# Kernel optimization log

Measured on AMD Instinct MI355X. Metric: run time of the kernel, lower is better.

## Reference

```python
import jax, jax.numpy as jnp
import numpy as np

B, CLS, BBOX, H, W = 64, 80, 2, 56, 56
TOPK = 2048
L_COORD, L_OBJ, L_NOOBJ = 5.0, 1.0, 0.5


def setup_inputs() -> dict:
    key = jax.random.key(0)
    ks = jax.random.split(key, 5)
    pred_cls = jax.random.normal(ks[0], (B, CLS, H, W), jnp.float32)
    pred_response = jax.random.uniform(ks[1], (B, BBOX, H, W), jnp.float32)
    pred_bboxes = jax.random.uniform(ks[2], (B, BBOX * 4, H, W), jnp.float32)
    label_cls = jax.random.uniform(ks[3], (B, CLS, H, W), jnp.float32)
    label_bboxes = jax.random.uniform(ks[4], (B, BBOX * 4, H, W), jnp.float32)
    # exactly TOPK positive cells so the data-dependent k is static
    rng = np.random.default_rng(0)
    flat = rng.choice(B * H * W, size=TOPK, replace=False)
    lr = np.zeros((B, BBOX, H, W), np.float32)
    b = flat // (H * W); rem = flat % (H * W)
    lr[b, :, rem // W, rem % W] = 1.0
    return {
        'pred_cls': pred_cls, 'pred_response': pred_response, 'pred_bboxes': pred_bboxes,
        'label_cls': label_cls, 'label_response': jnp.asarray(lr), 'label_bboxes': label_bboxes,
        'topk': TOPK,
    }


def _offset2box(box):
    # box: [N,4] (cx, cy, w, h) -> (x1, y1, x2, y2)
    x1 = box[:, 0] - box[:, 2] / 2
    y1 = box[:, 1] - box[:, 3] / 2
    return jnp.stack([x1, y1, x1 + box[:, 2], y1 + box[:, 3]], axis=1)


def _paired_iou(box1, box2):
    # elementwise (paired) IoU: box1, box2 [N,4] in (x1,y1,x2,y2)
    lt = jnp.maximum(box1[:, :2], box2[:, :2])
    rb = jnp.minimum(box1[:, 2:], box2[:, 2:])
    wh = jnp.clip(rb - lt, 0.0)
    inter = wh[:, 0] * wh[:, 1]
    a1 = (box1[:, 2] - box1[:, 0]) * (box1[:, 3] - box1[:, 1])
    a2 = (box2[:, 2] - box2[:, 0]) * (box2[:, 3] - box2[:, 1])
    return inter / (a1 + a2 - inter + 1e-4)


def reference(pred_cls, pred_response, pred_bboxes, label_cls, label_response, label_bboxes, topk):
    b_size, _, h, w = pred_cls.shape
    bbox_num = pred_response.shape[1]

    # --- positive cell selection (no grad) ---
    tmp = label_response.sum(axis=1)            # [B,H,W]
    flat = jnp.where(tmp < 0.5, 0.0, tmp).reshape(-1)
    _, idx = jax.lax.top_k(flat, topk)          # static k
    hw = h * w
    b_list = idx // hw
    rem = idx % hw
    y_list = rem // w
    x_list = rem % w

    # --- gather positives: [K, C] each ---
    t_resp = label_response[b_list, :, y_list, x_list]
    p_resp = pred_response[b_list, :, y_list, x_list]
    t_boxes = label_bboxes[b_list, :, y_list, x_list]    # [K, bbox*4]
    p_boxes = pred_bboxes[b_list, :, y_list, x_list]
    t_cls = label_cls[b_list, :, y_list, x_list]
    p_cls = pred_cls[b_list, :, y_list, x_list]

    loss_pos_cls = jnp.sum((p_cls - t_cls) ** 2)

    # --- IoU between paired boxes (no grad in original) ---
    t_off = t_boxes.reshape(-1, 4)
    p_off = p_boxes.reshape(-1, 4)
    iou = _paired_iou(_offset2box(t_off), _offset2box(p_off)).reshape(-1, bbox_num)
    iou = jax.lax.stop_gradient(iou)

    best = jnp.argmax(iou, axis=1)[:, None]     # [K,1]
    p_best_resp = jnp.take_along_axis(p_resp, best, axis=1)
    iou_best = jnp.take_along_axis(iou, best, axis=1)
    loss_pos_response = jnp.sum((p_best_resp - iou_best) ** 2)

    p_b = p_boxes.reshape(-1, bbox_num, 4)
    t_b = t_boxes.reshape(-1, bbox_num, 4)
    off_idx = best[:, :, None]                  # [K,1,1]
    p_sel = jnp.take_along_axis(p_b, jnp.broadcast_to(off_idx, (p_b.shape[0], 1, 4)), axis=1)
    t_sel = jnp.take_along_axis(t_b, jnp.broadcast_to(off_idx, (t_b.shape[0], 1, 4)), axis=1)
    loss_pos_offset = jnp.sum((p_sel - t_sel) ** 2)

    # --- negatives over the full map ---
    neg_mask = label_response < 1.0
    loss_neg_response = jnp.sum(jnp.where(neg_mask, (pred_response - label_response) ** 2, 0.0))

    pObj = loss_pos_response / b_size * L_OBJ
    nObj = loss_neg_response / b_size * L_NOOBJ
    cls_l = loss_pos_cls / b_size
    off_l = loss_pos_offset / b_size * L_COORD
    return jnp.stack([pObj, nObj, cls_l, off_l])
```

## Files before the change

kernel.cpp:

```cpp
#include <hip/hip_runtime.h>

#define BATCH 64
#define CLSN 80
#define BBOXN 2
#define HWN (56 * 56)
#define NCELLS (BATCH * HWN)
#define NTHR 256
#define NBLK (NCELLS / NTHR)


__global__ void yolo_fused_kernel(const float* __restrict__ pred_cls,
                                  const float* __restrict__ pred_resp,
                                  const float* __restrict__ pred_box,
                                  const float* __restrict__ label_cls,
                                  const float* __restrict__ label_resp,
                                  const float* __restrict__ label_box,
                                  float4* __restrict__ partials) {
    const int tid = threadIdx.x;
    const int i = blockIdx.x * NTHR + tid;
    const int b = i / HWN;
    const int yx = i - b * HWN;
    const int rbase = b * (BBOXN * HWN) + yx;

    const float l0 = label_resp[rbase];
    const float l1 = label_resp[rbase + HWN];
    const float p0 = pred_resp[rbase];
    const float p1 = pred_resp[rbase + HWN];

    float negAcc = 0.0f, clsAcc = 0.0f, respAcc = 0.0f, offAcc = 0.0f;
    if (l0 < 1.0f) { float d = p0 - l0; negAcc += d * d; }
    if (l1 < 1.0f) { float d = p1 - l1; negAcc += d * d; }

    const bool sel = (l0 + l1) >= 0.5f;

    if (sel) {
        const int bbase = b * (BBOXN * 4) * HWN + yx;
        float t[8], p[8];
        #pragma unroll
        for (int k = 0; k < 8; ++k) {
            t[k] = label_box[bbase + k * HWN];
            p[k] = pred_box[bbase + k * HWN];
        }
        float iou[2];
        #pragma unroll
        for (int bx = 0; bx < 2; ++bx) {
            float tx1 = t[bx * 4 + 0] - t[bx * 4 + 2] * 0.5f;
            float ty1 = t[bx * 4 + 1] - t[bx * 4 + 3] * 0.5f;
            float tx2 = tx1 + t[bx * 4 + 2];
            float ty2 = ty1 + t[bx * 4 + 3];
            float px1 = p[bx * 4 + 0] - p[bx * 4 + 2] * 0.5f;
            float py1 = p[bx * 4 + 1] - p[bx * 4 + 3] * 0.5f;
            float px2 = px1 + p[bx * 4 + 2];
            float py2 = py1 + p[bx * 4 + 3];
            float ltx = fmaxf(tx1, px1), lty = fmaxf(ty1, py1);
            float rbx = fminf(tx2, px2), rby = fminf(ty2, py2);
            float w_ = fmaxf(rbx - ltx, 0.0f), h_ = fmaxf(rby - lty, 0.0f);
            float inter = w_ * h_;
            float a1 = (tx2 - tx1) * (ty2 - ty1);
            float a2 = (px2 - px1) * (py2 - py1);
            iou[bx] = inter / (a1 + a2 - inter + 0.0001f);
        }
        const int best = (iou[1] > iou[0]) ? 1 : 0;
        const float pr = best ? p1 : p0;
        const float dr = pr - iou[best];
        respAcc = dr * dr;
        #pragma unroll
        for (int k = 0; k < 4; ++k) {
            float d2 = p[best * 4 + k] - t[best * 4 + k];
            offAcc += d2 * d2;
        }
    }

    const int lane = tid & 63;
    unsigned long long mask = __ballot(sel);
    while (mask) {
        const int srcLane = (int)__builtin_ctzll(mask);
        mask &= mask - 1;
        const int ci = __shfl(i, srcLane, 64);
        const int cb = ci / HWN;
        const int cyx = ci - cb * HWN;
        const int cbase = cb * (CLSN * HWN) + cyx;
        {
            const int ofs = cbase + lane * HWN;
            float d = pred_cls[ofs] - label_cls[ofs];
            clsAcc += d * d;
        }
        if (lane < CLSN - 64) {
            const int ofs = cbase + (64 + lane) * HWN;
            float d = pred_cls[ofs] - label_cls[ofs];
            clsAcc += d * d;
        }
    }

    #pragma unroll
    for (int o = 32; o > 0; o >>= 1) {
        negAcc  += __shfl_down(negAcc,  o, 64);
        clsAcc  += __shfl_down(clsAcc,  o, 64);
        respAcc += __shfl_down(respAcc, o, 64);
        offAcc  += __shfl_down(offAcc,  o, 64);
    }
    __shared__ float4 s[NTHR / 64];
    if ((tid & 63) == 0) s[tid >> 6] = make_float4(negAcc, clsAcc, respAcc, offAcc);
    __syncthreads();
    if (tid == 0) {
        float4 t = s[0];
        #pragma unroll
        for (int w = 1; w < NTHR / 64; ++w) {
            t.x += s[w].x; t.y += s[w].y; t.z += s[w].z; t.w += s[w].w;
        }
        partials[blockIdx.x] = t;
    }
}

__global__ void yolo_finalize_kernel(const float4* __restrict__ partials,
                                     float* __restrict__ out) {
    const int tid = threadIdx.x;
    double neg = 0.0, cls = 0.0, resp = 0.0, offs = 0.0;
    for (int k = tid; k < NBLK; k += NTHR) {
        float4 t = partials[k];
        neg += (double)t.x; cls += (double)t.y;
        resp += (double)t.z; offs += (double)t.w;
    }
    #pragma unroll
    for (int o = 32; o > 0; o >>= 1) {
        neg  += __shfl_down(neg,  o, 64);
        cls  += __shfl_down(cls,  o, 64);
        resp += __shfl_down(resp, o, 64);
        offs += __shfl_down(offs, o, 64);
    }
    __shared__ double s[4][NTHR / 64];
    const int w = tid >> 6;
    if ((tid & 63) == 0) { s[0][w] = neg; s[1][w] = cls; s[2][w] = resp; s[3][w] = offs; }
    __syncthreads();
    if (tid == 0) {
        double N = 0, C = 0, R = 0, O = 0;
        #pragma unroll
        for (int k = 0; k < NTHR / 64; ++k) {
            N += s[0][k]; C += s[1][k]; R += s[2][k]; O += s[3][k];
        }
        out[0] = (float)(R / (double)BATCH);
        out[1] = (float)(N / (double)BATCH * 0.5);
        out[2] = (float)(C / (double)BATCH);
        out[3] = (float)(O / (double)BATCH * 5.0);
    }
}

extern "C" void kernel_launch(void* const* d_in, const int* in_sizes, int n_in,
                              void* d_out, int out_size, void* d_ws, size_t ws_size,
                              hipStream_t stream) {
    const float* pred_cls   = (const float*)d_in[0];
    const float* pred_resp  = (const float*)d_in[1];
    const float* pred_box   = (const float*)d_in[2];
    const float* label_cls  = (const float*)d_in[3];
    const float* label_resp = (const float*)d_in[4];
    const float* label_box  = (const float*)d_in[5];

    float4* partials = (float4*)d_ws;
    float* out = (float*)d_out;

    yolo_fused_kernel<<<NBLK, NTHR, 0, stream>>>(
        pred_cls, pred_resp, pred_box, label_cls, label_resp, label_box, partials);

    yolo_finalize_kernel<<<1, NTHR, 0, stream>>>(partials, out);
}
```

Before: 15.81 us.

## Compact selected cells into shared list and gather class loss block-wide

Selected cells are no longer walked one at a time per wavefront with 80 class channels spread over lanes. They are appended to a shared-memory list with an atomic counter, and the whole block processes them six cells per iteration, with 240 threads each covering one (cell, class) pair and two loads issued per iteration. This raises memory-level parallelism and removes the per-wave serial loop and idle lanes. In exchange it adds two block barriers and a shared atomic, and the 128-entry list assumes at most 128 selected cells per block.

```diff
diff --git a/kernel.cpp b/kernel.cpp
--- a/kernel.cpp
+++ b/kernel.cpp
@@ -16,7 +16,12 @@
                                   const float* __restrict__ label_resp,
                                   const float* __restrict__ label_box,
                                   float4* __restrict__ partials) {
+    __shared__ int s_cnt;
+    __shared__ int s_list[128];
+
     const int tid = threadIdx.x;
+    if (tid == 0) s_cnt = 0;
+
     const int i = blockIdx.x * NTHR + tid;
     const int b = i / HWN;
     const int yx = i - b * HWN;
@@ -33,14 +38,46 @@
 
     const bool sel = (l0 + l1) >= 0.5f;
 
+    float t[8], p[8];
     if (sel) {
         const int bbase = b * (BBOXN * 4) * HWN + yx;
-        float t[8], p[8];
         #pragma unroll
         for (int k = 0; k < 8; ++k) {
             t[k] = label_box[bbase + k * HWN];
             p[k] = pred_box[bbase + k * HWN];
         }
+    }
+
+    __syncthreads();
+    if (sel) {
+        int slot = atomicAdd(&s_cnt, 1);
+        s_list[slot] = b * (CLSN * HWN) + yx;
+    }
+    __syncthreads();
+    const int nsel = s_cnt;
+
+    const int cslot = tid / CLSN;
+    const int ccls  = tid - cslot * CLSN;
+    const bool lane_ok = (tid < 3 * CLSN);
+    for (int r = 0; r < nsel; r += 6) {
+        const int sA = r + cslot;
+        const int sB = r + cslot + 3;
+        const bool aA = lane_ok && (sA < nsel);
+        const bool aB = lane_ok && (sB < nsel);
+        float pA = 0.0f, lA = 0.0f, pB = 0.0f, lB = 0.0f;
+        if (aA) {
+            const int ofs = s_list[sA] + ccls * HWN;
+            pA = pred_cls[ofs]; lA = label_cls[ofs];
+        }
+        if (aB) {
+            const int ofs = s_list[sB] + ccls * HWN;
+            pB = pred_cls[ofs]; lB = label_cls[ofs];
+        }
+        if (aA) { float d = pA - lA; clsAcc += d * d; }
+        if (aB) { float d = pB - lB; clsAcc += d * d; }
+    }
+
+    if (sel) {
         float iou[2];
         #pragma unroll
         for (int bx = 0; bx < 2; ++bx) {
@@ -71,27 +108,6 @@
         }
     }
 
-    const int lane = tid & 63;
-    unsigned long long mask = __ballot(sel);
-    while (mask) {
-        const int srcLane = (int)__builtin_ctzll(mask);
-        mask &= mask - 1;
-        const int ci = __shfl(i, srcLane, 64);
-        const int cb = ci / HWN;
-        const int cyx = ci - cb * HWN;
-        const int cbase = cb * (CLSN * HWN) + cyx;
-        {
-            const int ofs = cbase + lane * HWN;
-            float d = pred_cls[ofs] - label_cls[ofs];
-            clsAcc += d * d;
-        }
-        if (lane < CLSN - 64) {
-            const int ofs = cbase + (64 + lane) * HWN;
-            float d = pred_cls[ofs] - label_cls[ofs];
-            clsAcc += d * d;
-        }
-    }
-
     #pragma unroll
     for (int o = 32; o > 0; o >>= 1) {
         negAcc  += __shfl_down(negAcc,  o, 64);
@@ -103,12 +119,12 @@
     if ((tid & 63) == 0) s[tid >> 6] = make_float4(negAcc, clsAcc, respAcc, offAcc);
     __syncthreads();
     if (tid == 0) {
-        float4 t = s[0];
+        float4 tt = s[0];
         #pragma unroll
         for (int w = 1; w < NTHR / 64; ++w) {
-            t.x += s[w].x; t.y += s[w].y; t.z += s[w].z; t.w += s[w].w;
+            tt.x += s[w].x; tt.y += s[w].y; tt.z += s[w].z; tt.w += s[w].w;
         }
-        partials[blockIdx.x] = t;
+        partials[blockIdx.x] = tt;
     }
 }
 
```

New measurement: 15.35 us (median of 2 runs). 1.03x faster.
